# Kernel tuning notes

Measured on AMD Instinct MI355X. Metric: run time of the kernel, lower is better.

## Reference

```python
import jax, jax.numpy as jnp
import numpy as np

N = 8192
F_IN = 256
F_OUT = 128
SLOPE = 0.2
NEG_INF = -9000000000000000.0


def setup_inputs() -> dict:
    key = jax.random.key(0)
    k1, k2, k3, k4, k5 = jax.random.split(key, 5)
    x = jax.random.normal(k1, (N, F_IN), dtype=jnp.float32)
    adj = jax.random.randint(k2, (N, N), 0, 2).astype(jnp.float32)
    W = jax.random.normal(k3, (F_IN, F_OUT), dtype=jnp.float32) * (1.0 / np.sqrt(F_IN))
    a_src = jax.random.normal(k4, (F_OUT,), dtype=jnp.float32) * (1.0 / np.sqrt(F_OUT))
    a_dst = jax.random.normal(k5, (F_OUT,), dtype=jnp.float32) * (1.0 / np.sqrt(F_OUT))
    return {"x": x, "adj": adj, "W": W, "a_src": a_src, "a_dst": a_dst}


def reference(x, adj, W, a_src, a_dst):
    # h: (N, F_OUT)
    h = x @ W
    f_src = h @ a_src  # (N,)
    f_dst = h @ a_dst  # (N,)
    # additive attention scores: (N, N)
    e = f_src[:, None] + f_dst[None, :]
    e = jnp.where(e >= 0, e, SLOPE * e)  # leaky_relu
    e = jnp.where(adj > 0, e, NEG_INF)
    alpha = jax.nn.softmax(e, axis=1)  # (N, N)
    return alpha @ h  # (N, F_OUT)
```

## Files before the change

### kernel.cpp

```cpp
#include <hip/hip_runtime.h>
#include <hip/hip_bf16.h>

#define NN 8192
#define FIN 256
#define FO 128
#define ROWS 32
#define NCH 32
#define L2E 1.4426950408889634f
#define C2  0.28853900817779268f

typedef __bf16 bf16x8 __attribute__((ext_vector_type(8)));
typedef __bf16 bf16x2 __attribute__((ext_vector_type(2)));
typedef float  f32x4  __attribute__((ext_vector_type(4)));
typedef unsigned long long u64;
typedef u64 u64x2 __attribute__((ext_vector_type(2)));

__device__ __forceinline__ f32x4 ntload(const float* p) {
  return __builtin_nontemporal_load((const f32x4*)p);
}

__global__ __launch_bounds__(256) void k_proj(
    const float* __restrict__ x, const float* __restrict__ W,
    const float* __restrict__ a_src, const float* __restrict__ a_dst,
    __bf16* __restrict__ Bp, float* __restrict__ f_src, float* __restrict__ f_dst)
{
  __shared__ float xs[16 * FIN];
  __shared__ float fs[16], fd[16];
  const int tid = threadIdx.x;
  const int i0 = blockIdx.x * 16;

  const float4* xg = (const float4*)(x + (size_t)i0 * FIN);
  float4* xs4 = (float4*)xs;
  #pragma unroll
  for (int t = 0; t < 4; t++) xs4[tid + 256 * t] = xg[tid + 256 * t];
  if (tid < 16) { fs[tid] = 0.f; fd[tid] = 0.f; }
  __syncthreads();

  const int cq = tid & 31;
  const int rg = tid >> 5;
  const int c0 = cq * 4;
  const int r0 = rg * 2;
  float acc0[4] = {0.f,0.f,0.f,0.f};
  float acc1[4] = {0.f,0.f,0.f,0.f};
  const float* xr0 = xs + r0 * FIN;
  const float* xr1 = xs + (r0 + 1) * FIN;

  for (int k = 0; k < FIN; k += 4) {
    float4 xa = *(const float4*)(xr0 + k);
    float4 xb = *(const float4*)(xr1 + k);
    #pragma unroll
    for (int kk = 0; kk < 4; kk++) {
      float4 wv = *(const float4*)(W + (size_t)(k + kk) * FO + c0);
      float xav = ((const float*)&xa)[kk];
      float xbv = ((const float*)&xb)[kk];
      acc0[0] += xav * wv.x; acc0[1] += xav * wv.y;
      acc0[2] += xav * wv.z; acc0[3] += xav * wv.w;
      acc1[0] += xbv * wv.x; acc1[1] += xbv * wv.y;
      acc1[2] += xbv * wv.z; acc1[3] += xbv * wv.w;
    }
  }

  float4 as = *(const float4*)(a_src + c0);
  float4 ad = *(const float4*)(a_dst + c0);
  float ps0 = acc0[0]*as.x + acc0[1]*as.y + acc0[2]*as.z + acc0[3]*as.w;
  float ps1 = acc1[0]*as.x + acc1[1]*as.y + acc1[2]*as.z + acc1[3]*as.w;
  float pd0 = acc0[0]*ad.x + acc0[1]*ad.y + acc0[2]*ad.z + acc0[3]*ad.w;
  float pd1 = acc1[0]*ad.x + acc1[1]*ad.y + acc1[2]*ad.z + acc1[3]*ad.w;
  atomicAdd(&fs[r0],     ps0);
  atomicAdd(&fs[r0 + 1], ps1);
  atomicAdd(&fd[r0],     pd0);
  atomicAdd(&fd[r0 + 1], pd1);

  const int j0 = i0 + r0;
  const int kg = j0 >> 5;
  const int q  = (j0 >> 3) & 3;
  const int t0 = j0 & 7;
  #pragma unroll
  for (int c = 0; c < 4; c++) {
    const int n = c0 + c;
    bf16x2 v;
    v[0] = (__bf16)acc0[c];
    v[1] = (__bf16)acc1[c];
    size_t idx = ((size_t)(kg * 8 + (n >> 4)) * 64 + q * 16 + (n & 15)) * 8 + t0;
    *(bf16x2*)(Bp + idx) = v;
  }
  __syncthreads();
  if (tid < 16) { f_src[i0 + tid] = fs[tid]; f_dst[i0 + tid] = fd[tid]; }
}

__global__ __launch_bounds__(512, 2) void k_attn(
    const float* __restrict__ adj, const __bf16* __restrict__ Bp,
    const float* __restrict__ f_src, const float* __restrict__ f_dst,
    float* __restrict__ out)
{
  __shared__ __align__(16) float G1[NN];
  __shared__ __align__(16) float G2[NN];
  __shared__ __align__(16) u64 msk[2][ROWS][5];
  __shared__ float lsum[ROWS];

  const int tid = threadIdx.x;
  const int w = tid >> 6;
  const int lane = tid & 63;
  const int m = lane & 15;
  const int q = lane >> 4;
  const int i0 = blockIdx.x * ROWS;
  const int mt = w >> 2;
  const int nq = w & 3;

  const float* abase = adj + (size_t)(i0 + w * 4) * NN + lane * 4;
  f32x4 st0 = ntload(abase);
  f32x4 st1 = ntload(abase + NN);
  f32x4 st2 = ntload(abase + 2 * NN);
  f32x4 st3 = ntload(abase + 3 * NN);

  #pragma unroll
  for (int t = 0; t < NN / 512; ++t) {
    int j = t * 512 + tid;
    float d = f_dst[j];
    G1[j] = __builtin_amdgcn_exp2f(d * L2E);
    G2[j] = __builtin_amdgcn_exp2f(d * C2);
  }
  float s = f_src[i0 + mt * 16 + m];
  const float F1 = __builtin_amdgcn_exp2f(s * L2E);
  const float F2 = __builtin_amdgcn_exp2f(s * C2);

  f32x4 acc[2];
  acc[0] = (f32x4){0.f, 0.f, 0.f, 0.f};
  acc[1] = (f32x4){0.f, 0.f, 0.f, 0.f};
  float psum = 0.f;

  const int r0l = mt * 16 + m;

  for (int c = 0; c < NCH; ++c) {
    const int cur = c & 1;

    {
      u64 b0, b1, b2, b3;
      b0 = __ballot(st0[0] > 0.f); b1 = __ballot(st0[1] > 0.f);
      b2 = __ballot(st0[2] > 0.f); b3 = __ballot(st0[3] > 0.f);
      if (lane < 4) msk[cur][w*4+0][lane] = lane==0?b0:lane==1?b1:lane==2?b2:b3;
      b0 = __ballot(st1[0] > 0.f); b1 = __ballot(st1[1] > 0.f);
      b2 = __ballot(st1[2] > 0.f); b3 = __ballot(st1[3] > 0.f);
      if (lane < 4) msk[cur][w*4+1][lane] = lane==0?b0:lane==1?b1:lane==2?b2:b3;
      b0 = __ballot(st2[0] > 0.f); b1 = __ballot(st2[1] > 0.f);
      b2 = __ballot(st2[2] > 0.f); b3 = __ballot(st2[3] > 0.f);
      if (lane < 4) msk[cur][w*4+2][lane] = lane==0?b0:lane==1?b1:lane==2?b2:b3;
      b0 = __ballot(st3[0] > 0.f); b1 = __ballot(st3[1] > 0.f);
      b2 = __ballot(st3[2] > 0.f); b3 = __ballot(st3[3] > 0.f);
      if (lane < 4) msk[cur][w*4+3][lane] = lane==0?b0:lane==1?b1:lane==2?b2:b3;
    }

    if (c + 1 < NCH) {
      const float* nb = abase + (c + 1) * 256;
      st0 = ntload(nb);
      st1 = ntload(nb + NN);
      st2 = ntload(nb + 2 * NN);
      st3 = ntload(nb + 3 * NN);
    }
    __syncthreads();

    u64x2 Ma01 = *(const u64x2*)&msk[cur][r0l][0];
    u64x2 Ma23 = *(const u64x2*)&msk[cur][r0l][2];
    const u64 M0 = Ma01[0], M1 = Ma01[1], M2 = Ma23[0], M3 = Ma23[1];

    #pragma unroll
    for (int ss = 0; ss < 4; ++ss) {
      #pragma unroll
      for (int kg = 0; kg < 2; ++kg) {
        const int jj = c * 256 + ss * 64 + kg * 32 + q * 8;
        float4 u0 = *(const float4*)(G1 + jj);
        float4 u1 = *(const float4*)(G1 + jj + 4);
        float4 v0 = *(const float4*)(G2 + jj);
        float4 v1 = *(const float4*)(G2 + jj + 4);
        const unsigned b = ss * 16 + kg * 8 + q * 2;
        const unsigned e0 = (unsigned)(M0 >> b);
        const unsigned e1 = (unsigned)(M1 >> b);
        const unsigned e2 = (unsigned)(M2 >> b);
        const unsigned e3 = (unsigned)(M3 >> b);
        float p0 = (e0 & 1u) ? fmaxf(F1 * u0.x, F2 * v0.x) : 0.f;
        float p1 = (e1 & 1u) ? fmaxf(F1 * u0.y, F2 * v0.y) : 0.f;
        float p2 = (e2 & 1u) ? fmaxf(F1 * u0.z, F2 * v0.z) : 0.f;
        float p3 = (e3 & 1u) ? fmaxf(F1 * u0.w, F2 * v0.w) : 0.f;
        float p4 = (e0 & 2u) ? fmaxf(F1 * u1.x, F2 * v1.x) : 0.f;
        float p5 = (e1 & 2u) ? fmaxf(F1 * u1.y, F2 * v1.y) : 0.f;
        float p6 = (e2 & 2u) ? fmaxf(F1 * u1.z, F2 * v1.z) : 0.f;
        float p7 = (e3 & 2u) ? fmaxf(F1 * u1.w, F2 * v1.w) : 0.f;
        if (nq == 0)
          psum += ((p0 + p1) + (p2 + p3)) + ((p4 + p5) + (p6 + p7));
        bf16x8 a;
        a[0] = (__bf16)p0; a[1] = (__bf16)p1; a[2] = (__bf16)p2;
        a[3] = (__bf16)p3; a[4] = (__bf16)p4; a[5] = (__bf16)p5;
        a[6] = (__bf16)p6; a[7] = (__bf16)p7;

        const __bf16* bsrc = Bp + (size_t)(c * 8 + ss * 2 + kg) * 4096
                             + (size_t)(nq * 2) * 512 + lane * 8;
        bf16x8 bf0 = *(const bf16x8*)bsrc;
        bf16x8 bf1 = *(const bf16x8*)(bsrc + 512);
        acc[0] = __builtin_amdgcn_mfma_f32_16x16x32_bf16(a, bf0, acc[0], 0, 0, 0);
        acc[1] = __builtin_amdgcn_mfma_f32_16x16x32_bf16(a, bf1, acc[1], 0, 0, 0);
      }
    }
  }

  if (nq == 0) {
    float p = psum;
    p += __shfl_xor(p, 16);
    p += __shfl_xor(p, 32);
    if (lane < 16) lsum[mt * 16 + lane] = p;
  }
  __syncthreads();

  const int rr0 = mt * 16 + q * 4;
  #pragma unroll
  for (int r = 0; r < 4; ++r) {
    const float inv = 1.0f / lsum[rr0 + r];
    float* orow = out + (size_t)(i0 + rr0 + r) * FO + (nq * 2) * 16 + m;
    orow[0]  = acc[0][r] * inv;
    orow[16] = acc[1][r] * inv;
  }
}

extern "C" void kernel_launch(void* const* d_in, const int* in_sizes, int n_in,
                              void* d_out, int out_size, void* d_ws, size_t ws_size,
                              hipStream_t stream) {
  const float* x     = (const float*)d_in[0];
  const float* adj   = (const float*)d_in[1];
  const float* W     = (const float*)d_in[2];
  const float* a_src = (const float*)d_in[3];
  const float* a_dst = (const float*)d_in[4];
  float* out = (float*)d_out;

  char* ws = (char*)d_ws;
  __bf16* Bp   = (__bf16*)ws;
  float* f_src = (float*)(ws + 2097152);
  float* f_dst = (float*)(ws + 2097152 + 32768);

  hipLaunchKernelGGL(k_proj, dim3(512), dim3(256), 0, stream,
                     x, W, a_src, a_dst, Bp, f_src, f_dst);
  hipLaunchKernelGGL(k_attn, dim3(256), dim3(512), 0, stream,
                     adj, Bp, f_src, f_dst, out);
}
```

Baseline: 473.7 us.

## Warp-specialize attention kernel with dedicated producer waves for adjacency mask loading

Adds two producer wavefronts per block, each streaming 16 adjacency rows and packing them into LDS bitmasks two chunks ahead. The eight consumer waves only read masks and run the exp/MFMA work, syncing with the producers through barriers. This is meant to separate the bandwidth-bound adjacency stream from the compute so the two overlap better. In exchange, each producer lane holds 16 vector loads in flight, which raises register pressure, and the block grows to 640 threads without a min-blocks hint, which may reduce occupancy.

```diff
diff --git a/kernel.cpp b/kernel.cpp
--- a/kernel.cpp
+++ b/kernel.cpp
@@ -88,7 +88,7 @@
   if (tid < 16) { f_src[i0 + tid] = fs[tid]; f_dst[i0 + tid] = fd[tid]; }
 }
 
-__global__ __launch_bounds__(512, 2) void k_attn(
+__global__ __launch_bounds__(640) void k_attn(
     const float* __restrict__ adj, const __bf16* __restrict__ Bp,
     const float* __restrict__ f_src, const float* __restrict__ f_dst,
     float* __restrict__ out)
@@ -101,122 +101,143 @@
   const int tid = threadIdx.x;
   const int w = tid >> 6;
   const int lane = tid & 63;
-  const int m = lane & 15;
-  const int q = lane >> 4;
   const int i0 = blockIdx.x * ROWS;
-  const int mt = w >> 2;
-  const int nq = w & 3;
-
-  const float* abase = adj + (size_t)(i0 + w * 4) * NN + lane * 4;
-  f32x4 st0 = ntload(abase);
-  f32x4 st1 = ntload(abase + NN);
-  f32x4 st2 = ntload(abase + 2 * NN);
-  f32x4 st3 = ntload(abase + 3 * NN);
-
-  #pragma unroll
-  for (int t = 0; t < NN / 512; ++t) {
-    int j = t * 512 + tid;
-    float d = f_dst[j];
-    G1[j] = __builtin_amdgcn_exp2f(d * L2E);
-    G2[j] = __builtin_amdgcn_exp2f(d * C2);
-  }
-  float s = f_src[i0 + mt * 16 + m];
-  const float F1 = __builtin_amdgcn_exp2f(s * L2E);
-  const float F2 = __builtin_amdgcn_exp2f(s * C2);
-
-  f32x4 acc[2];
-  acc[0] = (f32x4){0.f, 0.f, 0.f, 0.f};
-  acc[1] = (f32x4){0.f, 0.f, 0.f, 0.f};
-  float psum = 0.f;
-
-  const int r0l = mt * 16 + m;
-
-  for (int c = 0; c < NCH; ++c) {
-    const int cur = c & 1;
-
-    {
-      u64 b0, b1, b2, b3;
-      b0 = __ballot(st0[0] > 0.f); b1 = __ballot(st0[1] > 0.f);
-      b2 = __ballot(st0[2] > 0.f); b3 = __ballot(st0[3] > 0.f);
-      if (lane < 4) msk[cur][w*4+0][lane] = lane==0?b0:lane==1?b1:lane==2?b2:b3;
-      b0 = __ballot(st1[0] > 0.f); b1 = __ballot(st1[1] > 0.f);
-      b2 = __ballot(st1[2] > 0.f); b3 = __ballot(st1[3] > 0.f);
-      if (lane < 4) msk[cur][w*4+1][lane] = lane==0?b0:lane==1?b1:lane==2?b2:b3;
-      b0 = __ballot(st2[0] > 0.f); b1 = __ballot(st2[1] > 0.f);
-      b2 = __ballot(st2[2] > 0.f); b3 = __ballot(st2[3] > 0.f);
-      if (lane < 4) msk[cur][w*4+2][lane] = lane==0?b0:lane==1?b1:lane==2?b2:b3;
-      b0 = __ballot(st3[0] > 0.f); b1 = __ballot(st3[1] > 0.f);
-      b2 = __ballot(st3[2] > 0.f); b3 = __ballot(st3[3] > 0.f);
-      if (lane < 4) msk[cur][w*4+3][lane] = lane==0?b0:lane==1?b1:lane==2?b2:b3;
-    }
-
-    if (c + 1 < NCH) {
-      const float* nb = abase + (c + 1) * 256;
-      st0 = ntload(nb);
-      st1 = ntload(nb + NN);
-      st2 = ntload(nb + 2 * NN);
-      st3 = ntload(nb + 3 * NN);
+
+  if (w >= 8) {
+    const int pw = w - 8;
+    const int prow0 = pw * 16;
+    const float* abase = adj + (size_t)(i0 + prow0) * NN + lane * 4;
+
+    f32x4 s0,s1,s2,s3,s4,s5,s6,s7,s8,s9,s10,s11,s12,s13,s14,s15;
+
+#define PLOAD(c) {                                                            \
+    const float* _b = abase + (size_t)(c) * 256;                              \
+    s0=ntload(_b);        s1=ntload(_b+NN);       s2=ntload(_b+2*NN);         \
+    s3=ntload(_b+3*NN);   s4=ntload(_b+4*NN);     s5=ntload(_b+5*NN);         \
+    s6=ntload(_b+6*NN);   s7=ntload(_b+7*NN);     s8=ntload(_b+8*NN);         \
+    s9=ntload(_b+9*NN);   s10=ntload(_b+10*NN);   s11=ntload(_b+11*NN);       \
+    s12=ntload(_b+12*NN); s13=ntload(_b+13*NN);   s14=ntload(_b+14*NN);       \
+    s15=ntload(_b+15*NN); }
+
+#define PROW(sv, slot, r) {                                                   \
+    u64 b0=__ballot(sv[0]>0.f), b1=__ballot(sv[1]>0.f);                       \
+    u64 b2=__ballot(sv[2]>0.f), b3=__ballot(sv[3]>0.f);                       \
+    if (lane < 4)                                                             \
+      msk[slot][prow0 + (r)][lane] = lane==0?b0:lane==1?b1:lane==2?b2:b3; }
+
+#define PPACK(slot) {                                                         \
+    PROW(s0,slot,0)  PROW(s1,slot,1)  PROW(s2,slot,2)  PROW(s3,slot,3)        \
+    PROW(s4,slot,4)  PROW(s5,slot,5)  PROW(s6,slot,6)  PROW(s7,slot,7)        \
+    PROW(s8,slot,8)  PROW(s9,slot,9)  PROW(s10,slot,10) PROW(s11,slot,11)     \
+    PROW(s12,slot,12) PROW(s13,slot,13) PROW(s14,slot,14) PROW(s15,slot,15) }
+
+    PLOAD(0)
+    PPACK(0)
+    PLOAD(1)
+    asm volatile("s_waitcnt lgkmcnt(0)" ::: "memory");
+    __builtin_amdgcn_s_barrier();
+    __builtin_amdgcn_sched_barrier(0);
+
+    for (int k = 0; k < NCH; ++k) {
+      if (k + 1 < NCH) {
+        PPACK((k + 1) & 1)
+        if (k + 2 < NCH) PLOAD(k + 2)
+      }
+      asm volatile("s_waitcnt lgkmcnt(0)" ::: "memory");
+      __builtin_amdgcn_s_barrier();
+      __builtin_amdgcn_sched_barrier(0);
     }
     __syncthreads();
-
-    u64x2 Ma01 = *(const u64x2*)&msk[cur][r0l][0];
-    u64x2 Ma23 = *(const u64x2*)&msk[cur][r0l][2];
-    const u64 M0 = Ma01[0], M1 = Ma01[1], M2 = Ma23[0], M3 = Ma23[1];
-
+#undef PLOAD
+#undef PROW
+#undef PPACK
+  } else {
+    const int m = lane & 15;
+    const int q = lane >> 4;
+    const int mt = w >> 2;
+    const int nq = w & 3;
+
+    const int ctid = tid;
     #pragma unroll
-    for (int ss = 0; ss < 4; ++ss) {
+    for (int t = 0; t < NN / 512; ++t) {
+      int j = t * 512 + ctid;
+      float d = f_dst[j];
+      G1[j] = __builtin_amdgcn_exp2f(d * L2E);
+      G2[j] = __builtin_amdgcn_exp2f(d * C2);
+    }
+    float s = f_src[i0 + mt * 16 + m];
+    const float F1 = __builtin_amdgcn_exp2f(s * L2E);
+    const float F2 = __builtin_amdgcn_exp2f(s * C2);
+
+    f32x4 acc0 = (f32x4){0.f, 0.f, 0.f, 0.f};
+    f32x4 acc1 = (f32x4){0.f, 0.f, 0.f, 0.f};
+    float psum = 0.f;
+    const int r0l = mt * 16 + m;
+
+    __syncthreads();
+
+    for (int c = 0; c < NCH; ++c) {
+      const int cur = c & 1;
+      u64x2 Ma01 = *(const u64x2*)&msk[cur][r0l][0];
+      u64x2 Ma23 = *(const u64x2*)&msk[cur][r0l][2];
+      const u64 M0 = Ma01[0], M1 = Ma01[1], M2 = Ma23[0], M3 = Ma23[1];
+
       #pragma unroll
-      for (int kg = 0; kg < 2; ++kg) {
-        const int jj = c * 256 + ss * 64 + kg * 32 + q * 8;
-        float4 u0 = *(const float4*)(G1 + jj);
-        float4 u1 = *(const float4*)(G1 + jj + 4);
-        float4 v0 = *(const float4*)(G2 + jj);
-        float4 v1 = *(const float4*)(G2 + jj + 4);
-        const unsigned b = ss * 16 + kg * 8 + q * 2;
-        const unsigned e0 = (unsigned)(M0 >> b);
-        const unsigned e1 = (unsigned)(M1 >> b);
-        const unsigned e2 = (unsigned)(M2 >> b);
-        const unsigned e3 = (unsigned)(M3 >> b);
-        float p0 = (e0 & 1u) ? fmaxf(F1 * u0.x, F2 * v0.x) : 0.f;
-        float p1 = (e1 & 1u) ? fmaxf(F1 * u0.y, F2 * v0.y) : 0.f;
-        float p2 = (e2 & 1u) ? fmaxf(F1 * u0.z, F2 * v0.z) : 0.f;
-        float p3 = (e3 & 1u) ? fmaxf(F1 * u0.w, F2 * v0.w) : 0.f;
-        float p4 = (e0 & 2u) ? fmaxf(F1 * u1.x, F2 * v1.x) : 0.f;
-        float p5 = (e1 & 2u) ? fmaxf(F1 * u1.y, F2 * v1.y) : 0.f;
-        float p6 = (e2 & 2u) ? fmaxf(F1 * u1.z, F2 * v1.z) : 0.f;
-        float p7 = (e3 & 2u) ? fmaxf(F1 * u1.w, F2 * v1.w) : 0.f;
-        if (nq == 0)
-          psum += ((p0 + p1) + (p2 + p3)) + ((p4 + p5) + (p6 + p7));
-        bf16x8 a;
-        a[0] = (__bf16)p0; a[1] = (__bf16)p1; a[2] = (__bf16)p2;
-        a[3] = (__bf16)p3; a[4] = (__bf16)p4; a[5] = (__bf16)p5;
-        a[6] = (__bf16)p6; a[7] = (__bf16)p7;
-
-        const __bf16* bsrc = Bp + (size_t)(c * 8 + ss * 2 + kg) * 4096
-                             + (size_t)(nq * 2) * 512 + lane * 8;
-        bf16x8 bf0 = *(const bf16x8*)bsrc;
-        bf16x8 bf1 = *(const bf16x8*)(bsrc + 512);
-        acc[0] = __builtin_amdgcn_mfma_f32_16x16x32_bf16(a, bf0, acc[0], 0, 0, 0);
-        acc[1] = __builtin_amdgcn_mfma_f32_16x16x32_bf16(a, bf1, acc[1], 0, 0, 0);
+      for (int ss = 0; ss < 4; ++ss) {
+        #pragma unroll
+        for (int kg = 0; kg < 2; ++kg) {
+          const int jj = c * 256 + ss * 64 + kg * 32 + q * 8;
+          float4 u0 = *(const float4*)(G1 + jj);
+          float4 u1 = *(const float4*)(G1 + jj + 4);
+          float4 v0 = *(const float4*)(G2 + jj);
+          float4 v1 = *(const float4*)(G2 + jj + 4);
+          const unsigned b = ss * 16 + kg * 8 + q * 2;
+          const unsigned e0 = (unsigned)(M0 >> b);
+          const unsigned e1 = (unsigned)(M1 >> b);
+          const unsigned e2 = (unsigned)(M2 >> b);
+          const unsigned e3 = (unsigned)(M3 >> b);
+          float p0 = (e0 & 1u) ? fmaxf(F1 * u0.x, F2 * v0.x) : 0.f;
+          float p1 = (e1 & 1u) ? fmaxf(F1 * u0.y, F2 * v0.y) : 0.f;
+          float p2 = (e2 & 1u) ? fmaxf(F1 * u0.z, F2 * v0.z) : 0.f;
+          float p3 = (e3 & 1u) ? fmaxf(F1 * u0.w, F2 * v0.w) : 0.f;
+          float p4 = (e0 & 2u) ? fmaxf(F1 * u1.x, F2 * v1.x) : 0.f;
+          float p5 = (e1 & 2u) ? fmaxf(F1 * u1.y, F2 * v1.y) : 0.f;
+          float p6 = (e2 & 2u) ? fmaxf(F1 * u1.z, F2 * v1.z) : 0.f;
+          float p7 = (e3 & 2u) ? fmaxf(F1 * u1.w, F2 * v1.w) : 0.f;
+          if (nq == 0)
+            psum += ((p0 + p1) + (p2 + p3)) + ((p4 + p5) + (p6 + p7));
+          bf16x8 a;
+          a[0] = (__bf16)p0; a[1] = (__bf16)p1; a[2] = (__bf16)p2;
+          a[3] = (__bf16)p3; a[4] = (__bf16)p4; a[5] = (__bf16)p5;
+          a[6] = (__bf16)p6; a[7] = (__bf16)p7;
+
+          const __bf16* bsrc = Bp + (size_t)(c * 8 + ss * 2 + kg) * 4096
+                               + (size_t)(nq * 2) * 512 + lane * 8;
+          bf16x8 bf0 = *(const bf16x8*)bsrc;
+          bf16x8 bf1 = *(const bf16x8*)(bsrc + 512);
+          acc0 = __builtin_amdgcn_mfma_f32_16x16x32_bf16(a, bf0, acc0, 0, 0, 0);
+          acc1 = __builtin_amdgcn_mfma_f32_16x16x32_bf16(a, bf1, acc1, 0, 0, 0);
+        }
       }
-    }
-  }
-
-  if (nq == 0) {
-    float p = psum;
-    p += __shfl_xor(p, 16);
-    p += __shfl_xor(p, 32);
-    if (lane < 16) lsum[mt * 16 + lane] = p;
-  }
-  __syncthreads();
-
-  const int rr0 = mt * 16 + q * 4;
-  #pragma unroll
-  for (int r = 0; r < 4; ++r) {
-    const float inv = 1.0f / lsum[rr0 + r];
-    float* orow = out + (size_t)(i0 + rr0 + r) * FO + (nq * 2) * 16 + m;
-    orow[0]  = acc[0][r] * inv;
-    orow[16] = acc[1][r] * inv;
+      __syncthreads();
+    }
+
+    if (nq == 0) {
+      float p = psum;
+      p += __shfl_xor(p, 16);
+      p += __shfl_xor(p, 32);
+      if (lane < 16) lsum[mt * 16 + lane] = p;
+    }
+    __syncthreads();
+
+    const int rr0 = mt * 16 + q * 4;
+    #pragma unroll
+    for (int r = 0; r < 4; ++r) {
+      const float inv = 1.0f / lsum[rr0 + r];
+      float* orow = out + (size_t)(i0 + rr0 + r) * FO + (nq * 2) * 16 + m;
+      orow[0]  = acc0[r] * inv;
+      orow[16] = acc1[r] * inv;
+    }
   }
 }
 
@@ -237,6 +258,6 @@
 
   hipLaunchKernelGGL(k_proj, dim3(512), dim3(256), 0, stream,
                      x, W, a_src, a_dst, Bp, f_src, f_dst);
-  hipLaunchKernelGGL(k_attn, dim3(256), dim3(512), 0, stream,
+  hipLaunchKernelGGL(k_attn, dim3(256), dim3(640), 0, stream,
                      adj, Bp, f_src, f_dst, out);
 }
```

Result: faster. 448.8 us (-5.2%).

## Split attention kernel into 16-wave producer/consumer stages with LDS-shared probabilities

Applied to the files above, without the earlier changes.

Doubles the attention block to 1024 threads. Each wave now computes only one 32-column slice of the masked exp probabilities and stores it to shared memory. The MFMA stage then splits the K dimension across two wave halves, with each wave handling a 16-column output slice, and reduces the partial accumulators through shared memory at the end. This removes the redundant per-wave recomputation of probabilities, which were previously done four times per row tile. It also prefetches adj two chunks ahead. In exchange it adds a second barrier per chunk, atomic row-sum accumulation, and a cross-wave reduction epilogue.

```diff
diff --git a/kernel.cpp b/kernel.cpp
--- a/kernel.cpp
+++ b/kernel.cpp
@@ -88,14 +88,16 @@
   if (tid < 16) { f_src[i0 + tid] = fs[tid]; f_dst[i0 + tid] = fd[tid]; }
 }
 
-__global__ __launch_bounds__(512, 2) void k_attn(
+__global__ __launch_bounds__(1024, 4) void k_attn(
     const float* __restrict__ adj, const __bf16* __restrict__ Bp,
     const float* __restrict__ f_src, const float* __restrict__ f_dst,
     float* __restrict__ out)
 {
   __shared__ __align__(16) float G1[NN];
   __shared__ __align__(16) float G2[NN];
-  __shared__ __align__(16) u64 msk[2][ROWS][5];
+  __shared__ __align__(16) u64 msk[ROWS][6];
+  __shared__ __align__(16) __bf16 af[2][8][64][8];
+  __shared__ __align__(16) float ared[2][8][64][4];
   __shared__ float lsum[ROWS];
 
   const int tid = threadIdx.x;
@@ -104,119 +106,139 @@
   const int m = lane & 15;
   const int q = lane >> 4;
   const int i0 = blockIdx.x * ROWS;
-  const int mt = w >> 2;
-  const int nq = w & 3;
-
-  const float* abase = adj + (size_t)(i0 + w * 4) * NN + lane * 4;
-  f32x4 st0 = ntload(abase);
-  f32x4 st1 = ntload(abase + NN);
-  f32x4 st2 = ntload(abase + 2 * NN);
-  f32x4 st3 = ntload(abase + 3 * NN);
+
+  const int mtA = w >> 3;
+  const int fA  = w & 7;
+  const int sqA = fA >> 1, kgA = fA & 1;
+  const int r0l = mtA * 16 + m;
+  const int h   = w >> 3;
+  const int nq8 = w & 7;
+
+  const float* abase = adj + (size_t)(i0 + 2 * w) * NN + lane * 4;
+  f32x4 sA0 = ntload(abase);
+  f32x4 sA1 = ntload(abase + NN);
+  f32x4 sB0 = ntload(abase + 256);
+  f32x4 sB1 = ntload(abase + NN + 256);
 
   #pragma unroll
-  for (int t = 0; t < NN / 512; ++t) {
-    int j = t * 512 + tid;
+  for (int t = 0; t < NN / 1024; ++t) {
+    int j = t * 1024 + tid;
     float d = f_dst[j];
     G1[j] = __builtin_amdgcn_exp2f(d * L2E);
     G2[j] = __builtin_amdgcn_exp2f(d * C2);
   }
-  float s = f_src[i0 + mt * 16 + m];
+  if (tid < ROWS) lsum[tid] = 0.f;
+  float s = f_src[i0 + mtA * 16 + m];
   const float F1 = __builtin_amdgcn_exp2f(s * L2E);
   const float F2 = __builtin_amdgcn_exp2f(s * C2);
 
-  f32x4 acc[2];
-  acc[0] = (f32x4){0.f, 0.f, 0.f, 0.f};
-  acc[1] = (f32x4){0.f, 0.f, 0.f, 0.f};
+  f32x4 accP0 = (f32x4){0.f, 0.f, 0.f, 0.f};
+  f32x4 accP1 = (f32x4){0.f, 0.f, 0.f, 0.f};
   float psum = 0.f;
 
-  const int r0l = mt * 16 + m;
-
-  for (int c = 0; c < NCH; ++c) {
-    const int cur = c & 1;
-
-    {
-      u64 b0, b1, b2, b3;
-      b0 = __ballot(st0[0] > 0.f); b1 = __ballot(st0[1] > 0.f);
-      b2 = __ballot(st0[2] > 0.f); b3 = __ballot(st0[3] > 0.f);
-      if (lane < 4) msk[cur][w*4+0][lane] = lane==0?b0:lane==1?b1:lane==2?b2:b3;
-      b0 = __ballot(st1[0] > 0.f); b1 = __ballot(st1[1] > 0.f);
-      b2 = __ballot(st1[2] > 0.f); b3 = __ballot(st1[3] > 0.f);
-      if (lane < 4) msk[cur][w*4+1][lane] = lane==0?b0:lane==1?b1:lane==2?b2:b3;
-      b0 = __ballot(st2[0] > 0.f); b1 = __ballot(st2[1] > 0.f);
-      b2 = __ballot(st2[2] > 0.f); b3 = __ballot(st2[3] > 0.f);
-      if (lane < 4) msk[cur][w*4+2][lane] = lane==0?b0:lane==1?b1:lane==2?b2:b3;
-      b0 = __ballot(st3[0] > 0.f); b1 = __ballot(st3[1] > 0.f);
-      b2 = __ballot(st3[2] > 0.f); b3 = __ballot(st3[3] > 0.f);
-      if (lane < 4) msk[cur][w*4+3][lane] = lane==0?b0:lane==1?b1:lane==2?b2:b3;
-    }
-
-    if (c + 1 < NCH) {
-      const float* nb = abase + (c + 1) * 256;
-      st0 = ntload(nb);
-      st1 = ntload(nb + NN);
-      st2 = ntload(nb + 2 * NN);
-      st3 = ntload(nb + 3 * NN);
-    }
-    __syncthreads();
-
-    u64x2 Ma01 = *(const u64x2*)&msk[cur][r0l][0];
-    u64x2 Ma23 = *(const u64x2*)&msk[cur][r0l][2];
-    const u64 M0 = Ma01[0], M1 = Ma01[1], M2 = Ma23[0], M3 = Ma23[1];
-
-    #pragma unroll
-    for (int ss = 0; ss < 4; ++ss) {
-      #pragma unroll
-      for (int kg = 0; kg < 2; ++kg) {
-        const int jj = c * 256 + ss * 64 + kg * 32 + q * 8;
-        float4 u0 = *(const float4*)(G1 + jj);
-        float4 u1 = *(const float4*)(G1 + jj + 4);
-        float4 v0 = *(const float4*)(G2 + jj);
-        float4 v1 = *(const float4*)(G2 + jj + 4);
-        const unsigned b = ss * 16 + kg * 8 + q * 2;
-        const unsigned e0 = (unsigned)(M0 >> b);
-        const unsigned e1 = (unsigned)(M1 >> b);
-        const unsigned e2 = (unsigned)(M2 >> b);
-        const unsigned e3 = (unsigned)(M3 >> b);
-        float p0 = (e0 & 1u) ? fmaxf(F1 * u0.x, F2 * v0.x) : 0.f;
-        float p1 = (e1 & 1u) ? fmaxf(F1 * u0.y, F2 * v0.y) : 0.f;
-        float p2 = (e2 & 1u) ? fmaxf(F1 * u0.z, F2 * v0.z) : 0.f;
-        float p3 = (e3 & 1u) ? fmaxf(F1 * u0.w, F2 * v0.w) : 0.f;
-        float p4 = (e0 & 2u) ? fmaxf(F1 * u1.x, F2 * v1.x) : 0.f;
-        float p5 = (e1 & 2u) ? fmaxf(F1 * u1.y, F2 * v1.y) : 0.f;
-        float p6 = (e2 & 2u) ? fmaxf(F1 * u1.z, F2 * v1.z) : 0.f;
-        float p7 = (e3 & 2u) ? fmaxf(F1 * u1.w, F2 * v1.w) : 0.f;
-        if (nq == 0)
-          psum += ((p0 + p1) + (p2 + p3)) + ((p4 + p5) + (p6 + p7));
-        bf16x8 a;
-        a[0] = (__bf16)p0; a[1] = (__bf16)p1; a[2] = (__bf16)p2;
-        a[3] = (__bf16)p3; a[4] = (__bf16)p4; a[5] = (__bf16)p5;
-        a[6] = (__bf16)p6; a[7] = (__bf16)p7;
-
-        const __bf16* bsrc = Bp + (size_t)(c * 8 + ss * 2 + kg) * 4096
-                             + (size_t)(nq * 2) * 512 + lane * 8;
-        bf16x8 bf0 = *(const bf16x8*)bsrc;
-        bf16x8 bf1 = *(const bf16x8*)(bsrc + 512);
-        acc[0] = __builtin_amdgcn_mfma_f32_16x16x32_bf16(a, bf0, acc[0], 0, 0, 0);
-        acc[1] = __builtin_amdgcn_mfma_f32_16x16x32_bf16(a, bf1, acc[1], 0, 0, 0);
-      }
-    }
-  }
-
-  if (nq == 0) {
+#define ITER(c, s0, s1)                                                       \
+  {                                                                           \
+        \
+    u64 b0 = __ballot(s0[0] > 0.f), b1 = __ballot(s0[1] > 0.f);               \
+    u64 b2 = __ballot(s0[2] > 0.f), b3 = __ballot(s0[3] > 0.f);               \
+    if (lane < 4) msk[2*w][lane]   = lane==0?b0:lane==1?b1:lane==2?b2:b3;     \
+    b0 = __ballot(s1[0] > 0.f); b1 = __ballot(s1[1] > 0.f);                   \
+    b2 = __ballot(s1[2] > 0.f); b3 = __ballot(s1[3] > 0.f);                   \
+    if (lane < 4) msk[2*w+1][lane] = lane==0?b0:lane==1?b1:lane==2?b2:b3;     \
+    __syncthreads();            \
+                                    \
+    {                                                                         \
+      u64x2 Ma = *(const u64x2*)&msk[r0l][0];                                 \
+      u64x2 Mb = *(const u64x2*)&msk[r0l][2];                                 \
+      const u64 M0 = Ma[0], M1 = Ma[1], M2 = Mb[0], M3 = Mb[1];               \
+      const int jj = (c) * 256 + sqA * 64 + kgA * 32 + q * 8;                 \
+      float4 u0 = *(const float4*)(G1 + jj);                                  \
+      float4 u1 = *(const float4*)(G1 + jj + 4);                              \
+      float4 v0 = *(const float4*)(G2 + jj);                                  \
+      float4 v1 = *(const float4*)(G2 + jj + 4);                              \
+      const unsigned b = sqA * 16 + kgA * 8 + q * 2;                          \
+      const unsigned e0 = (unsigned)(M0 >> b);                                \
+      const unsigned e1 = (unsigned)(M1 >> b);                                \
+      const unsigned e2 = (unsigned)(M2 >> b);                                \
+      const unsigned e3 = (unsigned)(M3 >> b);                                \
+      float p0 = (e0 & 1u) ? fmaxf(F1 * u0.x, F2 * v0.x) : 0.f;               \
+      float p1 = (e1 & 1u) ? fmaxf(F1 * u0.y, F2 * v0.y) : 0.f;               \
+      float p2 = (e2 & 1u) ? fmaxf(F1 * u0.z, F2 * v0.z) : 0.f;               \
+      float p3 = (e3 & 1u) ? fmaxf(F1 * u0.w, F2 * v0.w) : 0.f;               \
+      float p4 = (e0 & 2u) ? fmaxf(F1 * u1.x, F2 * v1.x) : 0.f;               \
+      float p5 = (e1 & 2u) ? fmaxf(F1 * u1.y, F2 * v1.y) : 0.f;               \
+      float p6 = (e2 & 2u) ? fmaxf(F1 * u1.z, F2 * v1.z) : 0.f;               \
+      float p7 = (e3 & 2u) ? fmaxf(F1 * u1.w, F2 * v1.w) : 0.f;               \
+      psum += ((p0 + p1) + (p2 + p3)) + ((p4 + p5) + (p6 + p7));              \
+      bf16x8 a;                                                               \
+      a[0] = (__bf16)p0; a[1] = (__bf16)p1; a[2] = (__bf16)p2;                \
+      a[3] = (__bf16)p3; a[4] = (__bf16)p4; a[5] = (__bf16)p5;                \
+      a[6] = (__bf16)p6; a[7] = (__bf16)p7;                                   \
+      *(bf16x8*)&af[mtA][fA][lane][0] = a;                                    \
+    }                                                                         \
+    __syncthreads();                                   \
+          \
+    {                                                                         \
+      const __bf16* bch = Bp + (size_t)((c) * 8 + h * 4) * 4096               \
+                          + (size_t)nq8 * 512 + lane * 8;                     \
+      bf16x8 bf0 = *(const bf16x8*)(bch);                                     \
+      bf16x8 bf1 = *(const bf16x8*)(bch + 4096);                              \
+      bf16x8 bf2 = *(const bf16x8*)(bch + 2 * 4096);                          \
+      bf16x8 bf3 = *(const bf16x8*)(bch + 3 * 4096);                          \
+      bf16x8 a00 = *(const bf16x8*)&af[0][h*4+0][lane][0];                    \
+      bf16x8 a10 = *(const bf16x8*)&af[1][h*4+0][lane][0];                    \
+      bf16x8 a01 = *(const bf16x8*)&af[0][h*4+1][lane][0];                    \
+      bf16x8 a11 = *(const bf16x8*)&af[1][h*4+1][lane][0];                    \
+      bf16x8 a02 = *(const bf16x8*)&af[0][h*4+2][lane][0];                    \
+      bf16x8 a12 = *(const bf16x8*)&af[1][h*4+2][lane][0];                    \
+      bf16x8 a03 = *(const bf16x8*)&af[0][h*4+3][lane][0];                    \
+      bf16x8 a13 = *(const bf16x8*)&af[1][h*4+3][lane][0];                    \
+      accP0 = __builtin_amdgcn_mfma_f32_16x16x32_bf16(a00, bf0, accP0, 0,0,0);\
+      accP1 = __builtin_amdgcn_mfma_f32_16x16x32_bf16(a10, bf0, accP1, 0,0,0);\
+      accP0 = __builtin_amdgcn_mfma_f32_16x16x32_bf16(a01, bf1, accP0, 0,0,0);\
+      accP1 = __builtin_amdgcn_mfma_f32_16x16x32_bf16(a11, bf1, accP1, 0,0,0);\
+      accP0 = __builtin_amdgcn_mfma_f32_16x16x32_bf16(a02, bf2, accP0, 0,0,0);\
+      accP1 = __builtin_amdgcn_mfma_f32_16x16x32_bf16(a12, bf2, accP1, 0,0,0);\
+      accP0 = __builtin_amdgcn_mfma_f32_16x16x32_bf16(a03, bf3, accP0, 0,0,0);\
+      accP1 = __builtin_amdgcn_mfma_f32_16x16x32_bf16(a13, bf3, accP1, 0,0,0);\
+    }                                                                         \
+        \
+    if ((c) + 2 < NCH) {                                                      \
+      s0 = ntload(abase + ((c) + 2) * 256);                                   \
+      s1 = ntload(abase + NN + ((c) + 2) * 256);                              \
+    }                                                                         \
+  }
+
+  for (int c = 0; c < NCH; c += 2) {
+    ITER(c, sA0, sA1)
+    ITER(c + 1, sB0, sB1)
+  }
+#undef ITER
+
+  {
     float p = psum;
     p += __shfl_xor(p, 16);
     p += __shfl_xor(p, 32);
-    if (lane < 16) lsum[mt * 16 + lane] = p;
+    if (lane < 16) atomicAdd(&lsum[mtA * 16 + lane], p);
+  }
+  if (h == 0) {
+    *(f32x4*)&ared[0][nq8][lane][0] = accP0;
+    *(f32x4*)&ared[1][nq8][lane][0] = accP1;
   }
   __syncthreads();
-
-  const int rr0 = mt * 16 + q * 4;
-  #pragma unroll
-  for (int r = 0; r < 4; ++r) {
-    const float inv = 1.0f / lsum[rr0 + r];
-    float* orow = out + (size_t)(i0 + rr0 + r) * FO + (nq * 2) * 16 + m;
-    orow[0]  = acc[0][r] * inv;
-    orow[16] = acc[1][r] * inv;
+  if (h == 1) {
+    f32x4 r0v = *(const f32x4*)&ared[0][nq8][lane][0];
+    f32x4 r1v = *(const f32x4*)&ared[1][nq8][lane][0];
+    f32x4 o0 = accP0 + r0v;
+    f32x4 o1 = accP1 + r1v;
+    #pragma unroll
+    for (int r = 0; r < 4; ++r) {
+      const int rr = q * 4 + r;
+      float inv0 = 1.0f / lsum[rr];
+      float inv1 = 1.0f / lsum[16 + rr];
+      out[(size_t)(i0 + rr) * FO + nq8 * 16 + m]      = o0[r] * inv0;
+      out[(size_t)(i0 + 16 + rr) * FO + nq8 * 16 + m] = o1[r] * inv1;
+    }
   }
 }
 
@@ -237,6 +259,6 @@
 
   hipLaunchKernelGGL(k_proj, dim3(512), dim3(256), 0, stream,
                      x, W, a_src, a_dst, Bp, f_src, f_dst);
-  hipLaunchKernelGGL(k_attn, dim3(256), dim3(512), 0, stream,
+  hipLaunchKernelGGL(k_attn, dim3(256), dim3(1024), 0, stream,
                      adj, Bp, f_src, f_dst, out);
 }
```

New measurement: 395.1 us. -16.6%, faster.
